# Performance work log

Measured on AMD Instinct MI355X. Metric: run time of the kernel, lower is better.

Reference implementation:

```python
import jax, jax.numpy as jnp
import numpy as np

N = 100000
E = 1600000
IN_N, IN_E = 128, 32
OUT_N, OUT_E = 64, 16
H = 4
NUM_CLASSES = 16
SLOPE = 0.2  # LeakyReLU negative slope (GAT default)


def _p(key, shape):
    return jax.random.normal(key, shape, dtype=jnp.float32) * 0.05


def setup_inputs() -> dict:
    key = jax.random.key(0)
    ks = jax.random.split(key, 20)
    inp = {
        'nfeat': jax.random.normal(ks[0], (N, IN_N), dtype=jnp.float32),
        'efeat': jax.random.normal(ks[1], (E, IN_E), dtype=jnp.float32),
        'src': jax.random.randint(ks[2], (E,), 0, N, dtype=jnp.int32),
        'dst': jax.random.randint(ks[3], (E,), 0, N, dtype=jnp.int32),
        # ---- conv1 params (EGATConv: in 128/32 -> out 64/16, 4 heads) ----
        'W1_ni': _p(ks[4], (IN_N, H * OUT_E)),
        'W1_fij': _p(ks[5], (IN_E, H * OUT_E)),
        'W1_nj': _p(ks[6], (IN_N, H * OUT_E)),
        'b1_edge': jnp.zeros((H * OUT_E,), jnp.float32),
        'W1_node': _p(ks[7], (IN_N, H * OUT_N)),
        'b1_node': jnp.zeros((H * OUT_N,), jnp.float32),
        'attn1': _p(ks[8], (H, OUT_E)),
        # ---- conv2 params (in 64/16 -> out num_classes / 1, 4 heads) ----
        'W2_ni': _p(ks[9], (OUT_N, H * 1)),
        'W2_fij': _p(ks[10], (OUT_E, H * 1)),
        'W2_nj': _p(ks[11], (OUT_N, H * 1)),
        'b2_edge': jnp.zeros((H * 1,), jnp.float32),
        'W2_node': _p(ks[12], (OUT_N, H * NUM_CLASSES)),
        'b2_node': jnp.zeros((H * NUM_CLASSES,), jnp.float32),
        'attn2': _p(ks[13], (H, 1)),
    }
    return inp


def egat_conv(nf, ef, src, dst, W_ni, W_fij, W_nj, b_edge, W_node, b_node, attn,
              heads, out_e, out_n):
    n = nf.shape[0]
    # edge feature projection: gather node projections onto edges
    f_ni = nf @ W_ni                                  # [N, H*oe]
    f_nj = nf @ W_nj                                  # [N, H*oe]
    f = f_ni[src] + (ef @ W_fij) + f_nj[dst] + b_edge  # [E, H*oe]
    f = jnp.where(f > 0, f, SLOPE * f)                 # LeakyReLU
    f = f.reshape(-1, heads, out_e)                    # [E, H, oe]
    # attention logits per head
    e = jnp.einsum('ehd,hd->eh', f, attn)              # [E, H]
    # segment softmax over destination neighborhoods
    m = jax.ops.segment_max(e, dst, num_segments=n)    # [N, H]
    a = jnp.exp(e - m[dst])
    s = jax.ops.segment_sum(a, dst, num_segments=n)    # [N, H]
    a = a / jnp.where(s == 0, 1.0, s)[dst]             # [E, H]
    # message passing: attention-weighted source features, scatter-sum to dst
    ft = (nf @ W_node + b_node).reshape(n, heads, out_n)  # [N, H, on]
    msg = ft[src] * a[:, :, None]                         # [E, H, on]
    out = jax.ops.segment_sum(msg, dst, num_segments=n)   # [N, H, on]
    return out, f


def reference(nfeat, efeat, src, dst,
              W1_ni, W1_fij, W1_nj, b1_edge, W1_node, b1_node, attn1,
              W2_ni, W2_fij, W2_nj, b2_edge, W2_node, b2_node, attn2):
    h, fe = egat_conv(nfeat, efeat, src, dst,
                      W1_ni, W1_fij, W1_nj, b1_edge, W1_node, b1_node, attn1,
                      H, OUT_E, OUT_N)
    # ReLU between layers; average heads so dims match conv2's declared inputs
    h = jax.nn.relu(h).mean(axis=1)    # [N, OUT_N]
    fe = jax.nn.relu(fe).mean(axis=1)  # [E, OUT_E]
    out, _ = egat_conv(h, fe, src, dst,
                       W2_ni, W2_fij, W2_nj, b2_edge, W2_node, b2_node, attn2,
                       H, 1, NUM_CLASSES)
    return out  # [N, H, NUM_CLASSES]
```

## Files before the change

kernel.cpp:

```cpp
#include <hip/hip_runtime.h>

#define SLOPE 0.2f
#define NPB 16

typedef float vf4 __attribute__((ext_vector_type(4)));
typedef float vf2 __attribute__((ext_vector_type(2)));
typedef _Float16 vh2 __attribute__((ext_vector_type(2)));
typedef _Float16 vh4 __attribute__((ext_vector_type(4)));
typedef _Float16 vh8 __attribute__((ext_vector_type(8)));

__device__ __forceinline__ float bcast_lane(float v, int k) {
    return __uint_as_float(__builtin_amdgcn_readlane(__float_as_uint(v), k));
}
__device__ __forceinline__ float dpp_sum16(float x) {
    x += __uint_as_float(__builtin_amdgcn_update_dpp(
        0, (int)__float_as_uint(x), 0x111, 0xf, 0xf, true));
    x += __uint_as_float(__builtin_amdgcn_update_dpp(
        0, (int)__float_as_uint(x), 0x112, 0xf, 0xf, true));
    x += __uint_as_float(__builtin_amdgcn_update_dpp(
        0, (int)__float_as_uint(x), 0x114, 0xf, 0xf, true));
    x += __uint_as_float(__builtin_amdgcn_update_dpp(
        0, (int)__float_as_uint(x), 0x118, 0xf, 0xf, true));
    return x;
}


__global__ __launch_bounds__(256) void k_deg_cvt(
    const int* __restrict__ dst, int* __restrict__ deg,
    const float* __restrict__ ef, _Float16* __restrict__ ef16, int E)
{
    const size_t i = (size_t)blockIdx.x * 256 + threadIdx.x;
    if (i < (size_t)E) atomicAdd(&deg[dst[i]], 1);
    const size_t b = i * 8;
    if (b < (size_t)E * 32) {
        const vf4 a0 = __builtin_nontemporal_load((const vf4*)(ef + b));
        const vf4 a1 = __builtin_nontemporal_load((const vf4*)(ef + b + 4));
        vh8 o;
        o[0] = (_Float16)a0.x; o[1] = (_Float16)a0.y;
        o[2] = (_Float16)a0.z; o[3] = (_Float16)a0.w;
        o[4] = (_Float16)a1.x; o[5] = (_Float16)a1.y;
        o[6] = (_Float16)a1.z; o[7] = (_Float16)a1.w;
        __builtin_nontemporal_store(o, (vh8*)(ef16 + b));
    }
}

__global__ __launch_bounds__(256) void k_scan1(
    const int* __restrict__ deg, int* __restrict__ bsum, int n)
{
    const int t = threadIdx.x;
    const int i0 = blockIdx.x * 1024 + t * 4;
    int s = 0;
#pragma unroll
    for (int j = 0; j < 4; j++) if (i0 + j < n) s += deg[i0 + j];
#pragma unroll
    for (int d = 1; d < 64; d <<= 1) s += __shfl_xor(s, d, 64);
    __shared__ int ws[4];
    if ((t & 63) == 0) ws[t >> 6] = s;
    __syncthreads();
    if (t == 0) bsum[blockIdx.x] = ws[0] + ws[1] + ws[2] + ws[3];
}

__global__ __launch_bounds__(64) void k_scan2(
    int* __restrict__ bsum, int* __restrict__ offs, int nb, int n)
{
    const int lane = threadIdx.x;
    int carry = 0;
    for (int base = 0; base < nb; base += 64) {
        const int i = base + lane;
        const int v = (i < nb) ? bsum[i] : 0;
        int x = v;
#pragma unroll
        for (int d = 1; d < 64; d <<= 1) {
            const int y = __shfl_up(x, d, 64);
            if (lane >= d) x += y;
        }
        if (i < nb) bsum[i] = carry + x - v;
        carry += __shfl(x, 63, 64);
    }
    if (lane == 0) offs[n] = carry;
}

__global__ __launch_bounds__(256) void k_scan3(
    const int* __restrict__ deg, const int* __restrict__ bsum,
    int* __restrict__ offs, int* __restrict__ cursor, int n)
{
    const int t = threadIdx.x;
    const int lane = t & 63, wid = t >> 6;
    const int i0 = blockIdx.x * 1024 + t * 4;
    const int d0 = (i0     < n) ? deg[i0]     : 0;
    const int d1 = (i0 + 1 < n) ? deg[i0 + 1] : 0;
    const int d2 = (i0 + 2 < n) ? deg[i0 + 2] : 0;
    const int d3 = (i0 + 3 < n) ? deg[i0 + 3] : 0;
    const int v = d0 + d1 + d2 + d3;
    int x = v;
#pragma unroll
    for (int d = 1; d < 64; d <<= 1) {
        const int y = __shfl_up(x, d, 64);
        if (lane >= d) x += y;
    }
    __shared__ int ws[4];
    if (lane == 63) ws[wid] = x;
    __syncthreads();
    int wbase = 0;
    for (int q = 0; q < wid; q++) wbase += ws[q];
    int excl = bsum[blockIdx.x] + wbase + (x - v);
    if (i0     < n) { offs[i0]     = excl; cursor[i0]     = excl; }
    excl += d0;
    if (i0 + 1 < n) { offs[i0 + 1] = excl; cursor[i0 + 1] = excl; }
    excl += d1;
    if (i0 + 2 < n) { offs[i0 + 2] = excl; cursor[i0 + 2] = excl; }
    excl += d2;
    if (i0 + 3 < n) { offs[i0 + 3] = excl; cursor[i0 + 3] = excl; }
}

__global__ __launch_bounds__(256) void k_scatter(
    const int* __restrict__ src, const int* __restrict__ dst,
    int* __restrict__ cursor, int2* __restrict__ se, int E)
{
    const int e = blockIdx.x * 256 + threadIdx.x;
    if (e >= E) return;
    const int p = atomicAdd(&cursor[dst[e]], 1);
    se[p] = make_int2(src[e], e);
}

__global__ __launch_bounds__(256) void k_nodeproj1(
    const float* __restrict__ nf, const float* __restrict__ Wni,
    const float* __restrict__ Wnj,
    _Float16* __restrict__ fni16, _Float16* __restrict__ fnj16,
    _Float16* __restrict__ nf16, int n)
{
    __shared__ float s[128][20];
    const int t = threadIdx.x;
    const int node0 = blockIdx.x * NPB;
    for (int i = 0; i < 8; i++) {
        const int idx = i * 256 + t;
        const int k = idx & 127, nl = idx >> 7;
        const int node = node0 + nl;
        const float v = (node < n) ? nf[(size_t)node * 128 + k] : 0.f;
        s[k][nl] = v;
        if (node < n) nf16[(size_t)node * 128 + k] = (_Float16)v;
    }
    __syncthreads();
    const int lane = t & 63;
    const int w4 = (t >> 6) * 4;
    float ai[4] = {0, 0, 0, 0}, aj[4] = {0, 0, 0, 0};
#pragma unroll 4
    for (int k = 0; k < 128; k++) {
        const float wi = Wni[(size_t)k * 64 + lane];
        const float wj = Wnj[(size_t)k * 64 + lane];
        const float4 sv = *(const float4*)&s[k][w4];
        const float sl[4] = {sv.x, sv.y, sv.z, sv.w};
#pragma unroll
        for (int nn = 0; nn < 4; nn++) {
            ai[nn] = fmaf(wi, sl[nn], ai[nn]);
            aj[nn] = fmaf(wj, sl[nn], aj[nn]);
        }
    }
#pragma unroll
    for (int nn = 0; nn < 4; nn++) {
        const int node = node0 + w4 + nn;
        if (node < n) {
            fni16[(size_t)node * 64 + lane] = (_Float16)ai[nn];
            fnj16[(size_t)node * 64 + lane] = (_Float16)aj[nn];
        }
    }
}

__global__ __launch_bounds__(256, 4) void k_l1(
    const int* __restrict__ offs, const int2* __restrict__ se,
    const _Float16* __restrict__ ef16,
    const _Float16* __restrict__ nf16, const _Float16* __restrict__ fni16,
    const _Float16* __restrict__ fnj16, const float* __restrict__ Wfij,
    const float* __restrict__ bedge, const float* __restrict__ attn,
    const float* __restrict__ Wfij2,
    _Float16* __restrict__ g2s, _Float16* __restrict__ zbuf, int n)
{
    const int lane = threadIdx.x & 63;
    const int node = __builtin_amdgcn_readfirstlane(blockIdx.x * 4 + (threadIdx.x >> 6));
    if (node >= n) return;
    const int beg = offs[node], end = offs[node + 1];
    const float fjb = (float)fnj16[(size_t)node * 64 + lane] + bedge[lane];
    const float at = attn[lane];
    const float w2f = Wfij2[(lane & 15) * 4 + (lane >> 4)];
    vh2 wf[16];
#pragma unroll
    for (int j = 0; j < 16; j++) {
        vh2 p;
        p.x = (_Float16)Wfij[(2 * j) * 64 + lane];
        p.y = (_Float16)Wfij[(2 * j + 1) * 64 + lane];
        wf[j] = p;
    }
#pragma unroll
    for (int j = 0; j < 16; j++) asm volatile("" : "+v"(wf[j]));

    float s0 = 0.f, s1 = 0.f, s2 = 0.f, s3 = 0.f;
    vf2 z0 = {0.f, 0.f}, z1 = {0.f, 0.f}, z2 = {0.f, 0.f}, z3 = {0.f, 0.f};

#define PAIR(u, j) (vh2){(u)[2 * (j)], (u)[2 * (j) + 1]}
    for (int base = beg; base < end; base += 64) {
        const int rem = end - base;
        const int cnt = (rem < 64) ? rem : 64;
        const int idx = base + ((lane < cnt) ? lane : (cnt - 1));
        const int2 sev = se[idx];
        const int spv = sev.x, edv = sev.y;
#pragma unroll 2
        for (int it = 0; it < cnt; ++it) {
            const int sp = __builtin_amdgcn_readlane(spv, it);
            const int ed = __builtin_amdgcn_readlane(edv, it);
            const vh8* __restrict__ er = (const vh8*)(ef16 + ((size_t)(unsigned)ed << 5));
            const vh8 u0 = __builtin_nontemporal_load(er + 0);
            const vh8 u1 = __builtin_nontemporal_load(er + 1);
            const vh8 u2 = __builtin_nontemporal_load(er + 2);
            const vh8 u3 = __builtin_nontemporal_load(er + 3);
            float f0 = (float)fni16[(size_t)(unsigned)sp * 64 + lane] + fjb;
            f0 = __builtin_amdgcn_fdot2(PAIR(u0, 0), wf[0],  f0, false);
            f0 = __builtin_amdgcn_fdot2(PAIR(u0, 1), wf[1],  f0, false);
            f0 = __builtin_amdgcn_fdot2(PAIR(u0, 2), wf[2],  f0, false);
            f0 = __builtin_amdgcn_fdot2(PAIR(u0, 3), wf[3],  f0, false);
            float f1 = __builtin_amdgcn_fdot2(PAIR(u1, 0), wf[4], 0.f, false);
            f1 = __builtin_amdgcn_fdot2(PAIR(u1, 1), wf[5],  f1, false);
            f1 = __builtin_amdgcn_fdot2(PAIR(u1, 2), wf[6],  f1, false);
            f1 = __builtin_amdgcn_fdot2(PAIR(u1, 3), wf[7],  f1, false);
            float f2 = __builtin_amdgcn_fdot2(PAIR(u2, 0), wf[8], 0.f, false);
            f2 = __builtin_amdgcn_fdot2(PAIR(u2, 1), wf[9],  f2, false);
            f2 = __builtin_amdgcn_fdot2(PAIR(u2, 2), wf[10], f2, false);
            f2 = __builtin_amdgcn_fdot2(PAIR(u2, 3), wf[11], f2, false);
            float f3 = __builtin_amdgcn_fdot2(PAIR(u3, 0), wf[12], 0.f, false);
            f3 = __builtin_amdgcn_fdot2(PAIR(u3, 1), wf[13], f3, false);
            f3 = __builtin_amdgcn_fdot2(PAIR(u3, 2), wf[14], f3, false);
            f3 = __builtin_amdgcn_fdot2(PAIR(u3, 3), wf[15], f3, false);
            const float f = (f0 + f1) + (f2 + f3);
            const float fl = (f > 0.f) ? f : SLOPE * f;
            float r = fmaxf(fl, 0.f);
            r += __shfl_xor(r, 16, 64);
            r += __shfl_xor(r, 32, 64);
            float g = dpp_sum16(0.25f * r * w2f);
            if ((lane & 15) == 15)
                g2s[(size_t)(base + it) * 4 + (lane >> 4)] = (_Float16)g;
            const float t = dpp_sum16(fl * at);
            const float ce = __expf(t);
            const float c0 = bcast_lane(ce, 15);
            const float c1 = bcast_lane(ce, 31);
            const float c2 = bcast_lane(ce, 47);
            const float c3 = bcast_lane(ce, 63);
            const vh2 nvh = *(const vh2*)(nf16 + (size_t)(unsigned)sp * 128 + lane * 2);
            const float nvx = (float)nvh.x, nvy = (float)nvh.y;
            s0 += c0; s1 += c1; s2 += c2; s3 += c3;
            z0.x = fmaf(c0, nvx, z0.x); z0.y = fmaf(c0, nvy, z0.y);
            z1.x = fmaf(c1, nvx, z1.x); z1.y = fmaf(c1, nvy, z1.y);
            z2.x = fmaf(c2, nvx, z2.x); z2.y = fmaf(c2, nvy, z2.y);
            z3.x = fmaf(c3, nvx, z3.x); z3.y = fmaf(c3, nvy, z3.y);
        }
    }
#undef PAIR
    const float i0 = (s0 > 0.f) ? 1.f / s0 : 0.f;
    const float i1 = (s1 > 0.f) ? 1.f / s1 : 0.f;
    const float i2 = (s2 > 0.f) ? 1.f / s2 : 0.f;
    const float i3 = (s3 > 0.f) ? 1.f / s3 : 0.f;
    _Float16* zb = zbuf + (size_t)node * 512;
    vh2 o;
    o.x = (_Float16)(z0.x * i0); o.y = (_Float16)(z0.y * i0);
    *(vh2*)(zb + 0   + lane * 2) = o;
    o.x = (_Float16)(z1.x * i1); o.y = (_Float16)(z1.y * i1);
    *(vh2*)(zb + 128 + lane * 2) = o;
    o.x = (_Float16)(z2.x * i2); o.y = (_Float16)(z2.y * i2);
    *(vh2*)(zb + 256 + lane * 2) = o;
    o.x = (_Float16)(z3.x * i3); o.y = (_Float16)(z3.y * i3);
    *(vh2*)(zb + 384 + lane * 2) = o;
}

__global__ __launch_bounds__(256) void k_zproj(
    const _Float16* __restrict__ zbuf, const int* __restrict__ offs,
    const float* __restrict__ Wnode, const float* __restrict__ bnode,
    _Float16* __restrict__ hbuf16, int n)
{
    __shared__ float s[512][20];
    const int t = threadIdx.x;
    const int node0 = blockIdx.x * NPB;
    for (int i = 0; i < 16; i++) {
        const int idx = i * 256 + t;
        const int nl = idx >> 8, kk = (idx & 255) * 2;
        const int node = node0 + nl;
        vh2 v = {0.f, 0.f};
        if (node < n) v = *(const vh2*)(zbuf + (size_t)node * 512 + kk);
        s[kk][nl]     = (float)v.x;
        s[kk + 1][nl] = (float)v.y;
    }
    __syncthreads();
    const int lane = t & 63;
    const int w4 = (t >> 6) * 4;
    bool zf[4];
    float hb[4] = {0, 0, 0, 0};
#pragma unroll
    for (int nn = 0; nn < 4; nn++) {
        const int node = node0 + w4 + nn;
        zf[nn] = (node < n) && (offs[node] < offs[node + 1]);
    }
#pragma unroll
    for (int h = 0; h < 4; h++) {
        float acc[4];
        const float bv = bnode[h * 64 + lane];
#pragma unroll
        for (int nn = 0; nn < 4; nn++) acc[nn] = zf[nn] ? bv : 0.f;
#pragma unroll 4
        for (int k = 0; k < 128; k++) {
            const float wv = Wnode[(size_t)k * 256 + h * 64 + lane];
            const float4 sv = *(const float4*)&s[h * 128 + k][w4];
            acc[0] = fmaf(wv, sv.x, acc[0]);
            acc[1] = fmaf(wv, sv.y, acc[1]);
            acc[2] = fmaf(wv, sv.z, acc[2]);
            acc[3] = fmaf(wv, sv.w, acc[3]);
        }
#pragma unroll
        for (int nn = 0; nn < 4; nn++) hb[nn] += fmaxf(acc[nn], 0.f);
    }
#pragma unroll
    for (int nn = 0; nn < 4; nn++) {
        const int node = node0 + w4 + nn;
        if (node < n) hbuf16[(size_t)node * 64 + lane] = (_Float16)(0.25f * hb[nn]);
    }
}

__global__ __launch_bounds__(256) void k_nodeproj2(
    const _Float16* __restrict__ hbuf16, const float* __restrict__ Wni,
    const float* __restrict__ Wnj, const float* __restrict__ Wnode,
    const float* __restrict__ bnode,
    float* __restrict__ fni2, float* __restrict__ fnj2,
    _Float16* __restrict__ ft2h, int n)
{
    __shared__ float sh[4][64];
    const int lane = threadIdx.x & 63, w = threadIdx.x >> 6;
    const int node = blockIdx.x * 4 + w;
    const int nc = (node < n) ? node : (n - 1);
    const float v = (float)hbuf16[(size_t)nc * 64 + lane];
    sh[w][lane] = v;
    __syncthreads();
    float acc = bnode[lane];
#pragma unroll 4
    for (int k = 0; k < 64; k++) acc = fmaf(sh[w][k], Wnode[k * 64 + lane], acc);
    float pi[4], pj[4];
#pragma unroll
    for (int h = 0; h < 4; h++) { pi[h] = v * Wni[lane * 4 + h]; pj[h] = v * Wnj[lane * 4 + h]; }
#pragma unroll
    for (int mk = 1; mk < 64; mk <<= 1) {
#pragma unroll
        for (int h = 0; h < 4; h++) {
            pi[h] += __shfl_xor(pi[h], mk, 64);
            pj[h] += __shfl_xor(pj[h], mk, 64);
        }
    }
    if (node < n) {
        ft2h[(size_t)node * 64 + lane] = (_Float16)acc;
        if (lane == 0) {
            *(float4*)(fni2 + (size_t)node * 4) = make_float4(pi[0], pi[1], pi[2], pi[3]);
            *(float4*)(fnj2 + (size_t)node * 4) = make_float4(pj[0], pj[1], pj[2], pj[3]);
        }
    }
}

__global__ __launch_bounds__(256) void k_l2(
    const int* __restrict__ offs, const int2* __restrict__ se,
    const _Float16* __restrict__ g2s, const float* __restrict__ fni2,
    const float* __restrict__ fnj2, const _Float16* __restrict__ ft2h,
    const float* __restrict__ bedge2, const float* __restrict__ attn2,
    float* __restrict__ out, int n)
{
    const int lane = threadIdx.x & 63;
    const int node = __builtin_amdgcn_readfirstlane(blockIdx.x * 4 + (threadIdx.x >> 6));
    if (node >= n) return;
    const int beg = offs[node], end = offs[node + 1];
    const int h = lane >> 4;
    const float base_ = fnj2[(size_t)node * 4 + h] + bedge2[h];
    const float at = attn2[h];
    float s = 0.f, acc = 0.f;
    for (int base = beg; base < end; base += 64) {
        const int rem = end - base;
        const int cnt = (rem < 64) ? rem : 64;
        const int idx = base + ((lane < cnt) ? lane : (cnt - 1));
        const int spv = se[idx].x;
#pragma unroll 4
        for (int it = 0; it < cnt; ++it) {
            const int sp = __builtin_amdgcn_readlane(spv, it);
            const int p = base + it;
            const vh4 gq = *(const vh4*)(g2s + (size_t)p * 4);
            const float4 fq = *(const float4*)(fni2 + (size_t)(unsigned)sp * 4);
            const float gh = (float)((h == 0) ? gq.x : (h == 1) ? gq.y : (h == 2) ? gq.z : gq.w);
            const float fh = (h == 0) ? fq.x : (h == 1) ? fq.y : (h == 2) ? fq.z : fq.w;
            const float f = base_ + fh + gh;
            const float fl = (f > 0.f) ? f : SLOPE * f;
            const float c = __expf(fl * at);
            s += c;
            const float ftv = (float)ft2h[(size_t)(unsigned)sp * 64 + lane];
            acc = fmaf(c, ftv, acc);
        }
    }
    out[(size_t)node * 64 + lane] = (s > 0.f) ? acc / s : 0.f;
}

extern "C" void kernel_launch(void* const* d_in, const int* in_sizes, int n_in,
                              void* d_out, int out_size, void* d_ws, size_t ws_size,
                              hipStream_t stream)
{
    const float* nfeat  = (const float*)d_in[0];
    const float* efeat  = (const float*)d_in[1];
    const int*   src    = (const int*)d_in[2];
    const int*   dst    = (const int*)d_in[3];
    const float* W1ni   = (const float*)d_in[4];
    const float* W1fij  = (const float*)d_in[5];
    const float* W1nj   = (const float*)d_in[6];
    const float* b1e    = (const float*)d_in[7];
    const float* W1node = (const float*)d_in[8];
    const float* b1n    = (const float*)d_in[9];
    const float* attn1  = (const float*)d_in[10];
    const float* W2ni   = (const float*)d_in[11];
    const float* W2fij  = (const float*)d_in[12];
    const float* W2nj   = (const float*)d_in[13];
    const float* b2e    = (const float*)d_in[14];
    const float* W2node = (const float*)d_in[15];
    const float* b2n    = (const float*)d_in[16];
    const float* attn2  = (const float*)d_in[17];
    const int n = in_sizes[0] / 128;
    const int E = in_sizes[2];
    float* out = (float*)d_out;

    char* w = (char*)d_ws;
    auto alloc = [&](size_t bytes) {
        char* p = w; w += (bytes + 255) & ~(size_t)255; return p;
    };
    _Float16* ef16  = (_Float16*)alloc((size_t)E * 32 * 2);
    _Float16* zbuf  = (_Float16*)alloc((size_t)n * 512 * 2);
    _Float16* g2s   = (_Float16*)alloc((size_t)E * 4 * 2);
    _Float16* fni16 = (_Float16*)alloc((size_t)n * 64 * 2);
    _Float16* fnj16 = (_Float16*)alloc((size_t)n * 64 * 2);
    _Float16* nf16  = (_Float16*)alloc((size_t)n * 128 * 2);
    _Float16* ft2h  = (_Float16*)alloc((size_t)n * 64 * 2);
    _Float16* hbuf16= (_Float16*)alloc((size_t)n * 64 * 2);
    int*      deg   = (int*)alloc((size_t)n * 4);
    int*      offs  = (int*)alloc((size_t)(n + 1) * 4);
    int*      curs  = (int*)alloc((size_t)n * 4);
    int2*     se    = (int2*)alloc((size_t)E * 8);
    float*    fni2  = (float*)alloc((size_t)n * 4 * 4);
    float*    fnj2  = (float*)alloc((size_t)n * 4 * 4);
    const int nb = (n + 1023) / 1024;
    int*      bsum  = (int*)alloc((size_t)nb * 4);

    hipMemsetAsync(deg, 0, (size_t)n * 4, stream);
    const int cvtBlocks = (int)(((size_t)E * 4 + 255) / 256);
    k_deg_cvt<<<cvtBlocks, 256, 0, stream>>>(dst, deg, efeat, ef16, E);
    k_scan1<<<nb, 256, 0, stream>>>(deg, bsum, n);
    k_scan2<<<1, 64, 0, stream>>>(bsum, offs, nb, n);
    k_scan3<<<nb, 256, 0, stream>>>(deg, bsum, offs, curs, n);
    k_scatter<<<(E + 255) / 256, 256, 0, stream>>>(src, dst, curs, se, E);

    k_nodeproj1<<<(n + NPB - 1) / NPB, 256, 0, stream>>>(
        nfeat, W1ni, W1nj, fni16, fnj16, nf16, n);
    k_l1<<<(n + 3) / 4, 256, 0, stream>>>(offs, se, ef16, nf16,
                                          fni16, fnj16, W1fij, b1e, attn1,
                                          W2fij, g2s, zbuf, n);
    k_zproj<<<(n + NPB - 1) / NPB, 256, 0, stream>>>(zbuf, offs, W1node, b1n,
                                                     hbuf16, n);
    k_nodeproj2<<<(n + 3) / 4, 256, 0, stream>>>(hbuf16, W2ni, W2nj, W2node, b2n,
                                                 fni2, fnj2, ft2h, n);
    k_l2<<<(n + 3) / 4, 256, 0, stream>>>(offs, se, g2s, fni2, fnj2, ft2h,
                                          b2e, attn2, out, n);
}
```

Measured before the change: 1.053 ms.

## Permute fp16 edge features into dst-sorted CSR order during conversion

The float-to-fp16 edge feature conversion now writes each edge row at its CSR position (recorded by the scatter kernel), so k_l1 reads edge features contiguously by position instead of gathering by original edge id. The int2 (src, edge) array is split into a plain src array plus a pos array. This turns random 64-byte gathers in the main layer-1 loop into sequential reads, at the cost of a scattered write in the conversion kernel, an extra launch and an extra pos array.

```diff
diff --git a/kernel.cpp b/kernel.cpp
--- a/kernel.cpp
+++ b/kernel.cpp
@@ -25,23 +25,11 @@
 }
 
 
-__global__ __launch_bounds__(256) void k_deg_cvt(
-    const int* __restrict__ dst, int* __restrict__ deg,
-    const float* __restrict__ ef, _Float16* __restrict__ ef16, int E)
-{
-    const size_t i = (size_t)blockIdx.x * 256 + threadIdx.x;
-    if (i < (size_t)E) atomicAdd(&deg[dst[i]], 1);
-    const size_t b = i * 8;
-    if (b < (size_t)E * 32) {
-        const vf4 a0 = __builtin_nontemporal_load((const vf4*)(ef + b));
-        const vf4 a1 = __builtin_nontemporal_load((const vf4*)(ef + b + 4));
-        vh8 o;
-        o[0] = (_Float16)a0.x; o[1] = (_Float16)a0.y;
-        o[2] = (_Float16)a0.z; o[3] = (_Float16)a0.w;
-        o[4] = (_Float16)a1.x; o[5] = (_Float16)a1.y;
-        o[6] = (_Float16)a1.z; o[7] = (_Float16)a1.w;
-        __builtin_nontemporal_store(o, (vh8*)(ef16 + b));
-    }
+__global__ __launch_bounds__(256) void k_deg(
+    const int* __restrict__ dst, int* __restrict__ deg, int E)
+{
+    const int e = blockIdx.x * 256 + threadIdx.x;
+    if (e < E) atomicAdd(&deg[dst[e]], 1);
 }
 
 __global__ __launch_bounds__(256) void k_scan1(
@@ -115,12 +103,35 @@
 
 __global__ __launch_bounds__(256) void k_scatter(
     const int* __restrict__ src, const int* __restrict__ dst,
-    int* __restrict__ cursor, int2* __restrict__ se, int E)
+    int* __restrict__ cursor, int* __restrict__ srcs, int* __restrict__ pos,
+    int E)
 {
     const int e = blockIdx.x * 256 + threadIdx.x;
     if (e >= E) return;
     const int p = atomicAdd(&cursor[dst[e]], 1);
-    se[p] = make_int2(src[e], e);
+    srcs[p] = src[e];
+    pos[e] = p;
+}
+
+__global__ __launch_bounds__(256) void k_cvt(
+    const float* __restrict__ ef, const int* __restrict__ pos,
+    _Float16* __restrict__ ef16s, int E)
+{
+    const int e = blockIdx.x * 256 + threadIdx.x;
+    if (e >= E) return;
+    const vf4* __restrict__ er = (const vf4*)(ef + (size_t)e * 32);
+    _Float16* __restrict__ op = ef16s + ((size_t)(unsigned)pos[e] << 5);
+#pragma unroll
+    for (int i = 0; i < 4; i++) {
+        const vf4 a0 = __builtin_nontemporal_load(er + 2 * i);
+        const vf4 a1 = __builtin_nontemporal_load(er + 2 * i + 1);
+        vh8 o;
+        o[0] = (_Float16)a0.x; o[1] = (_Float16)a0.y;
+        o[2] = (_Float16)a0.z; o[3] = (_Float16)a0.w;
+        o[4] = (_Float16)a1.x; o[5] = (_Float16)a1.y;
+        o[6] = (_Float16)a1.z; o[7] = (_Float16)a1.w;
+        *(vh8*)(op + i * 8) = o;
+    }
 }
 
 __global__ __launch_bounds__(256) void k_nodeproj1(
@@ -167,8 +178,8 @@
 }
 
 __global__ __launch_bounds__(256, 4) void k_l1(
-    const int* __restrict__ offs, const int2* __restrict__ se,
-    const _Float16* __restrict__ ef16,
+    const int* __restrict__ offs, const int* __restrict__ srcs,
+    const _Float16* __restrict__ ef16s,
     const _Float16* __restrict__ nf16, const _Float16* __restrict__ fni16,
     const _Float16* __restrict__ fnj16, const float* __restrict__ Wfij,
     const float* __restrict__ bedge, const float* __restrict__ attn,
@@ -201,17 +212,16 @@
         const int rem = end - base;
         const int cnt = (rem < 64) ? rem : 64;
         const int idx = base + ((lane < cnt) ? lane : (cnt - 1));
-        const int2 sev = se[idx];
-        const int spv = sev.x, edv = sev.y;
+        const int spv = srcs[idx];
 #pragma unroll 2
         for (int it = 0; it < cnt; ++it) {
             const int sp = __builtin_amdgcn_readlane(spv, it);
-            const int ed = __builtin_amdgcn_readlane(edv, it);
-            const vh8* __restrict__ er = (const vh8*)(ef16 + ((size_t)(unsigned)ed << 5));
-            const vh8 u0 = __builtin_nontemporal_load(er + 0);
-            const vh8 u1 = __builtin_nontemporal_load(er + 1);
-            const vh8 u2 = __builtin_nontemporal_load(er + 2);
-            const vh8 u3 = __builtin_nontemporal_load(er + 3);
+            const int p = base + it;
+            const vh8* __restrict__ er = (const vh8*)(ef16s + ((size_t)p << 5));
+            const vh8 u0 = er[0];
+            const vh8 u1 = er[1];
+            const vh8 u2 = er[2];
+            const vh8 u3 = er[3];
             float f0 = (float)fni16[(size_t)(unsigned)sp * 64 + lane] + fjb;
             f0 = __builtin_amdgcn_fdot2(PAIR(u0, 0), wf[0],  f0, false);
             f0 = __builtin_amdgcn_fdot2(PAIR(u0, 1), wf[1],  f0, false);
@@ -236,7 +246,7 @@
             r += __shfl_xor(r, 32, 64);
             float g = dpp_sum16(0.25f * r * w2f);
             if ((lane & 15) == 15)
-                g2s[(size_t)(base + it) * 4 + (lane >> 4)] = (_Float16)g;
+                g2s[(size_t)p * 4 + (lane >> 4)] = (_Float16)g;
             const float t = dpp_sum16(fl * at);
             const float ce = __expf(t);
             const float c0 = bcast_lane(ce, 15);
@@ -359,7 +369,7 @@
 }
 
 __global__ __launch_bounds__(256) void k_l2(
-    const int* __restrict__ offs, const int2* __restrict__ se,
+    const int* __restrict__ offs, const int* __restrict__ srcs,
     const _Float16* __restrict__ g2s, const float* __restrict__ fni2,
     const float* __restrict__ fnj2, const _Float16* __restrict__ ft2h,
     const float* __restrict__ bedge2, const float* __restrict__ attn2,
@@ -377,7 +387,7 @@
         const int rem = end - base;
         const int cnt = (rem < 64) ? rem : 64;
         const int idx = base + ((lane < cnt) ? lane : (cnt - 1));
-        const int spv = se[idx].x;
+        const int spv = srcs[idx];
 #pragma unroll 4
         for (int it = 0; it < cnt; ++it) {
             const int sp = __builtin_amdgcn_readlane(spv, it);
@@ -427,7 +437,7 @@
     auto alloc = [&](size_t bytes) {
         char* p = w; w += (bytes + 255) & ~(size_t)255; return p;
     };
-    _Float16* ef16  = (_Float16*)alloc((size_t)E * 32 * 2);
+    _Float16* ef16s = (_Float16*)alloc((size_t)E * 32 * 2);
     _Float16* zbuf  = (_Float16*)alloc((size_t)n * 512 * 2);
     _Float16* g2s   = (_Float16*)alloc((size_t)E * 4 * 2);
     _Float16* fni16 = (_Float16*)alloc((size_t)n * 64 * 2);
@@ -438,29 +448,30 @@
     int*      deg   = (int*)alloc((size_t)n * 4);
     int*      offs  = (int*)alloc((size_t)(n + 1) * 4);
     int*      curs  = (int*)alloc((size_t)n * 4);
-    int2*     se    = (int2*)alloc((size_t)E * 8);
+    int*      srcs  = (int*)alloc((size_t)E * 4);
+    int*      pos   = (int*)alloc((size_t)E * 4);
     float*    fni2  = (float*)alloc((size_t)n * 4 * 4);
     float*    fnj2  = (float*)alloc((size_t)n * 4 * 4);
     const int nb = (n + 1023) / 1024;
     int*      bsum  = (int*)alloc((size_t)nb * 4);
 
     hipMemsetAsync(deg, 0, (size_t)n * 4, stream);
-    const int cvtBlocks = (int)(((size_t)E * 4 + 255) / 256);
-    k_deg_cvt<<<cvtBlocks, 256, 0, stream>>>(dst, deg, efeat, ef16, E);
+    k_deg<<<(E + 255) / 256, 256, 0, stream>>>(dst, deg, E);
     k_scan1<<<nb, 256, 0, stream>>>(deg, bsum, n);
     k_scan2<<<1, 64, 0, stream>>>(bsum, offs, nb, n);
     k_scan3<<<nb, 256, 0, stream>>>(deg, bsum, offs, curs, n);
-    k_scatter<<<(E + 255) / 256, 256, 0, stream>>>(src, dst, curs, se, E);
+    k_scatter<<<(E + 255) / 256, 256, 0, stream>>>(src, dst, curs, srcs, pos, E);
+    k_cvt<<<(E + 255) / 256, 256, 0, stream>>>(efeat, pos, ef16s, E);
 
     k_nodeproj1<<<(n + NPB - 1) / NPB, 256, 0, stream>>>(
         nfeat, W1ni, W1nj, fni16, fnj16, nf16, n);
-    k_l1<<<(n + 3) / 4, 256, 0, stream>>>(offs, se, ef16, nf16,
+    k_l1<<<(n + 3) / 4, 256, 0, stream>>>(offs, srcs, ef16s, nf16,
                                           fni16, fnj16, W1fij, b1e, attn1,
                                           W2fij, g2s, zbuf, n);
     k_zproj<<<(n + NPB - 1) / NPB, 256, 0, stream>>>(zbuf, offs, W1node, b1n,
                                                      hbuf16, n);
     k_nodeproj2<<<(n + 3) / 4, 256, 0, stream>>>(hbuf16, W2ni, W2nj, W2node, b2n,
                                                  fni2, fnj2, ft2h, n);
-    k_l2<<<(n + 3) / 4, 256, 0, stream>>>(offs, se, g2s, fni2, fnj2, ft2h,
+    k_l2<<<(n + 3) / 4, 256, 0, stream>>>(offs, srcs, g2s, fni2, fnj2, ft2h,
                                           b2e, attn2, out, n);
 }
```

After: 1.159 ms. 1.1x slower.
